# Kernel optimization log

Hardware: AMD Instinct MI355X
Metric: run time of the kernel (lower is better)

Reference implementation:

```python
import jax, jax.numpy as jnp
import numpy as np
from jax import lax

D_MODEL = 1024
EXPAND = 2
D_INNER = EXPAND * D_MODEL          # 2048
HEADDIM = 64
NHEADS = D_INNER // HEADDIM         # 32
D_STATE = 128
D_CONV = 4
NGROUPS = 1
CONV_DIM = D_INNER + 2 * NGROUPS * D_STATE   # 2304
D_IN_PROJ = 2 * D_INNER + 2 * NGROUPS * D_STATE + NHEADS  # 4384
EPS = 1e-5
BSZ, SEQ = 4, 1024


def _layer_norm(x):
    mu = jnp.mean(x, -1, keepdims=True)
    v = jnp.var(x, -1, keepdims=True)
    return (x - mu) * lax.rsqrt(v + EPS)


def _smart_flip(X, mask):
    # reverse only the non-padded prefix of each sequence
    B, L, _ = X.shape
    lengths = jnp.sum(~mask, axis=1)                     # (B,)
    r = jnp.arange(L)[None, :]                           # (1,L)
    pos = jnp.where(r < lengths[:, None], lengths[:, None] - 1 - r, r)
    return jnp.take_along_axis(X, pos[:, :, None], axis=1)


def _mamba2(u, in_proj_w, conv_w, conv_b, dt_bias, A_log, D, norm_w, out_proj_w):
    B, L, _ = u.shape
    zxbcdt = jnp.einsum('bld,ed->ble', u, in_proj_w)     # (B,L,D_IN_PROJ)
    z = zxbcdt[..., :D_INNER]
    xBC = zxbcdt[..., D_INNER:D_INNER + CONV_DIM]
    dt = zxbcdt[..., D_INNER + CONV_DIM:]                # (B,L,H)
    dt = jax.nn.softplus(dt + dt_bias)
    # causal depthwise conv1d over time, then SiLU
    xc = jnp.transpose(xBC, (0, 2, 1))                   # (B,C,L)
    xc = jnp.pad(xc, ((0, 0), (0, 0), (D_CONV - 1, 0)))
    xc = lax.conv_general_dilated(xc, conv_w.reshape(CONV_DIM, 1, D_CONV), (1,), 'VALID',
                                  feature_group_count=CONV_DIM)
    xBC = jax.nn.silu(jnp.transpose(xc + conv_b[None, :, None], (0, 2, 1)))
    x = xBC[..., :D_INNER].reshape(B, L, NHEADS, HEADDIM)
    Bmat = xBC[..., D_INNER:D_INNER + D_STATE]           # (B,L,N)  (ngroups=1)
    Cmat = xBC[..., D_INNER + D_STATE:]                  # (B,L,N)
    A = -jnp.exp(A_log)                                  # (H,)
    dA = jnp.exp(dt * A)                                 # (B,L,H)

    def step(h, inp):
        dA_t, dt_t, x_t, B_t, C_t = inp
        # h: (B,H,P,N)
        h = h * dA_t[:, :, None, None] + (dt_t[:, :, None] * x_t)[..., None] * B_t[:, None, None, :]
        y = jnp.einsum('bhpn,bn->bhp', h, C_t)
        return h, y

    h0 = jnp.zeros((B, NHEADS, HEADDIM, D_STATE), u.dtype)
    xs = (jnp.moveaxis(dA, 1, 0), jnp.moveaxis(dt, 1, 0), jnp.moveaxis(x, 1, 0),
          jnp.moveaxis(Bmat, 1, 0), jnp.moveaxis(Cmat, 1, 0))
    _, ys = lax.scan(step, h0, xs)                       # (L,B,H,P)
    y = jnp.moveaxis(ys, 0, 1) + D[None, None, :, None] * x
    y = y.reshape(B, L, D_INNER)
    g = y * jax.nn.silu(z)                               # gated RMSNorm (norm_before_gate=False)
    y = g * lax.rsqrt(jnp.mean(g * g, -1, keepdims=True) + EPS) * norm_w
    return jnp.einsum('ble,de->bld', y, out_proj_w)


def setup_inputs() -> dict:
    key = jax.random.key(0)
    ks = jax.random.split(key, 16)
    dt_f = jax.random.uniform(ks[4], (NHEADS,), minval=0.001, maxval=0.1)
    dt_r = jax.random.uniform(ks[10], (NHEADS,), minval=0.001, maxval=0.1)
    inv_softplus = lambda d: d + jnp.log(-jnp.expm1(-d))
    return {
        'hidden_states': jax.random.normal(ks[0], (BSZ, SEQ, D_MODEL), jnp.float32),
        'src_key_padding_mask': jnp.zeros((BSZ, SEQ), jnp.bool_),
        'in_proj_w': jax.random.normal(ks[1], (D_IN_PROJ, D_MODEL), jnp.float32) / np.sqrt(D_MODEL),
        'out_proj_w': jax.random.normal(ks[2], (D_MODEL, D_INNER), jnp.float32) / np.sqrt(D_INNER),
        'conv_w_f': jax.random.normal(ks[3], (CONV_DIM, D_CONV), jnp.float32) / np.sqrt(D_CONV),
        'conv_b_f': jnp.zeros((CONV_DIM,), jnp.float32),
        'dt_bias_f': inv_softplus(dt_f),
        'A_log_f': jnp.log(jax.random.uniform(ks[5], (NHEADS,), minval=1.0, maxval=16.0)),
        'D_f': jnp.ones((NHEADS,), jnp.float32),
        'norm_w_f': jnp.ones((D_INNER,), jnp.float32),
        'conv_w_r': jax.random.normal(ks[9], (CONV_DIM, D_CONV), jnp.float32) / np.sqrt(D_CONV),
        'conv_b_r': jnp.zeros((CONV_DIM,), jnp.float32),
        'dt_bias_r': inv_softplus(dt_r),
        'A_log_r': jnp.log(jax.random.uniform(ks[11], (NHEADS,), minval=1.0, maxval=16.0)),
        'D_r': jnp.ones((NHEADS,), jnp.float32),
        'norm_w_r': jnp.ones((D_INNER,), jnp.float32),
    }


def reference(hidden_states, src_key_padding_mask, in_proj_w, out_proj_w,
              conv_w_f, conv_b_f, dt_bias_f, A_log_f, D_f, norm_w_f,
              conv_w_r, conv_b_r, dt_bias_r, A_log_r, D_r, norm_w_r):
    h = _layer_norm(hidden_states)
    out = _mamba2(h, in_proj_w, conv_w_f, conv_b_f, dt_bias_f, A_log_f, D_f, norm_w_f, out_proj_w)
    rev = _smart_flip(h, src_key_padding_mask)
    out_rev = _mamba2(rev, in_proj_w, conv_w_r, conv_b_r, dt_bias_r, A_log_r, D_r, norm_w_r, out_proj_w)
    out_rev = _smart_flip(out_rev, src_key_padding_mask)
    out = (out + out_rev) / 2
    return _layer_norm(out)
```

## Files before the change

### kernel.cpp

```cpp
#include <hip/hip_runtime.h>


#define BSZ 4
#define SEQ 1024
#define DMODEL 1024
#define DINNER 2048
#define NHEADS 32
#define HEADDIM 64
#define DSTATE 128
#define CONVDIM 2304
#define DPROJ 4384
#define DPROJ_PAD 4480
#define NTOK (BSZ*SEQ)
#define EPSF 1e-5f
#define CH 32
#define NCHK (SEQ/CH)

typedef float f32x4 __attribute__((ext_vector_type(4)));
typedef __bf16 bf16x8 __attribute__((ext_vector_type(8)));

__device__ __forceinline__ unsigned short f2bf(float f) {
  unsigned int x = __float_as_uint(f);
  unsigned int r = (x + 0x7fffu + ((x >> 16) & 1u)) >> 16;
  return (unsigned short)r;
}
__device__ __forceinline__ float bf2f(unsigned short u) {
  return __uint_as_float(((unsigned int)u) << 16);
}

__device__ __forceinline__ void async_load16(const void* g, void* l) {
  __builtin_amdgcn_global_load_lds(
      (const __attribute__((address_space(1))) void*)g,
      (__attribute__((address_space(3))) void*)l, 16, 0, 0);
}

#define W1N (DPROJ_PAD * DMODEL)
#define W2N (DMODEL * DINNER)
__global__ void k_convert(const float* __restrict__ w1, const float* __restrict__ w2,
                          unsigned short* __restrict__ o1, unsigned short* __restrict__ o2) {
  int idx = blockIdx.x * 256 + threadIdx.x;
  if (idx < W1N) {
    int row = idx >> 10, col = idx & 1023;
    float v = (row < DPROJ) ? w1[(size_t)row * DMODEL + col] : 0.f;
    o1[idx] = f2bf(v);
  } else {
    int k = idx - W1N;
    o2[k] = f2bf(w2[k]);
  }
}
__global__ void k_lengths(const unsigned char* __restrict__ mask, int* __restrict__ lengths) {
  int b = blockIdx.x, tid = threadIdx.x;
  int cnt = 0;
  for (int k = 0; k < 4; ++k)
    cnt += (mask[(size_t)b * SEQ + tid + k * 256] == 0) ? 1 : 0;
  for (int o = 32; o > 0; o >>= 1) cnt += __shfl_down(cnt, o);
  __shared__ int red[4];
  if ((tid & 63) == 0) red[tid >> 6] = cnt;
  __syncthreads();
  if (tid == 0) lengths[b] = red[0] + red[1] + red[2] + red[3];
}

__global__ __launch_bounds__(256) void k_ln_bf16(const float* __restrict__ in,
                                                 unsigned short* __restrict__ out) {
  int row = blockIdx.x, tid = threadIdx.x;
  float4 v = ((const float4*)(in + (size_t)row * DMODEL))[tid];
  float s = v.x + v.y + v.z + v.w;
  float ss = v.x * v.x + v.y * v.y + v.z * v.z + v.w * v.w;
  for (int o = 32; o > 0; o >>= 1) { s += __shfl_down(s, o); ss += __shfl_down(ss, o); }
  __shared__ float red[8];
  if ((tid & 63) == 0) { red[tid >> 6] = s; red[4 + (tid >> 6)] = ss; }
  __syncthreads();
  s = red[0] + red[1] + red[2] + red[3];
  ss = red[4] + red[5] + red[6] + red[7];
  float mu = s * (1.f / DMODEL);
  float var = ss * (1.f / DMODEL) - mu * mu;
  float rs = rsqrtf(var + EPSF);
  ushort4 o;
  o.x = f2bf((v.x - mu) * rs); o.y = f2bf((v.y - mu) * rs);
  o.z = f2bf((v.z - mu) * rs); o.w = f2bf((v.w - mu) * rs);
  ((ushort4*)(out + (size_t)row * DMODEL))[tid] = o;
}

__global__ __launch_bounds__(256) void k_ln_out(const unsigned short* __restrict__ in,
                                                float* __restrict__ out) {
  int row = blockIdx.x, tid = threadIdx.x;
  ushort4 u = ((const ushort4*)(in + (size_t)row * DMODEL))[tid];
  float4 v;
  v.x = bf2f(u.x); v.y = bf2f(u.y); v.z = bf2f(u.z); v.w = bf2f(u.w);
  float s = v.x + v.y + v.z + v.w;
  float ss = v.x * v.x + v.y * v.y + v.z * v.z + v.w * v.w;
  for (int o = 32; o > 0; o >>= 1) { s += __shfl_down(s, o); ss += __shfl_down(ss, o); }
  __shared__ float red[8];
  if ((tid & 63) == 0) { red[tid >> 6] = s; red[4 + (tid >> 6)] = ss; }
  __syncthreads();
  s = red[0] + red[1] + red[2] + red[3];
  ss = red[4] + red[5] + red[6] + red[7];
  float mu = s * (1.f / DMODEL);
  float var = ss * (1.f / DMODEL) - mu * mu;
  float rs = rsqrtf(var + EPSF);
  float4 o;
  o.x = (v.x - mu) * rs; o.y = (v.y - mu) * rs;
  o.z = (v.z - mu) * rs; o.w = (v.w - mu) * rs;
  ((float4*)(out + (size_t)row * DMODEL))[tid] = o;
}

__global__ __launch_bounds__(256) void k_gemm_bt_h(const unsigned short* __restrict__ A,
                                                   const unsigned short* __restrict__ B,
                                                   unsigned short* __restrict__ C,
                                                   int K, int lda, int ldb, int ldc) {
  __shared__ unsigned short Asm[2][128 * 32];
  __shared__ unsigned short Bsm[2][128 * 32];
  const int tid = threadIdx.x;
  const int lane = tid & 63;
  const int w = tid >> 6;
  const int wm = w >> 1, wn = w & 1;
  const long m0 = (long)blockIdx.x * 128;
  const long n0 = (long)blockIdx.y * 128;

  const int sr = lane >> 2;
  const int sc = (lane & 3) * 8;
  const unsigned short* gA0 = A + (m0 + (w * 2 + 0) * 16 + sr) * (long)lda + sc;
  const unsigned short* gA1 = A + (m0 + (w * 2 + 1) * 16 + sr) * (long)lda + sc;
  const unsigned short* gB0 = B + (n0 + (w * 2 + 0) * 16 + sr) * (long)ldb + sc;
  const unsigned short* gB1 = B + (n0 + (w * 2 + 1) * 16 + sr) * (long)ldb + sc;

  f32x4 acc[4][4] = {};
  const int q8 = (lane >> 4) * 8;
  const int r16 = lane & 15;

  for (int k0 = 0; k0 < K; k0 += 64) {
#pragma unroll
    for (int h = 0; h < 2; ++h) {
      const int ko = k0 + h * 32;
      async_load16(gA0 + ko, Asm[h] + (w * 2 + 0) * 512);
      async_load16(gA1 + ko, Asm[h] + (w * 2 + 1) * 512);
      async_load16(gB0 + ko, Bsm[h] + (w * 2 + 0) * 512);
      async_load16(gB1 + ko, Bsm[h] + (w * 2 + 1) * 512);
    }
    __syncthreads();
#pragma unroll
    for (int h = 0; h < 2; ++h) {
      bf16x8 af[4], bfr[4];
#pragma unroll
      for (int i = 0; i < 4; ++i)
        af[i] = *reinterpret_cast<const bf16x8*>(Asm[h] + (wm * 64 + i * 16 + r16) * 32 + q8);
#pragma unroll
      for (int j = 0; j < 4; ++j)
        bfr[j] = *reinterpret_cast<const bf16x8*>(Bsm[h] + (wn * 64 + j * 16 + r16) * 32 + q8);
#pragma unroll
      for (int i = 0; i < 4; ++i)
#pragma unroll
        for (int j = 0; j < 4; ++j)
          acc[i][j] = __builtin_amdgcn_mfma_f32_16x16x32_bf16(af[i], bfr[j], acc[i][j], 0, 0, 0);
    }
    __syncthreads();
  }
  const int q = lane >> 4, cn = lane & 15;
#pragma unroll
  for (int i = 0; i < 4; ++i)
#pragma unroll
    for (int j = 0; j < 4; ++j) {
      long crow = m0 + wm * 64 + i * 16 + q * 4;
      long ccol = n0 + wn * 64 + j * 16 + cn;
#pragma unroll
      for (int r = 0; r < 4; ++r)
        C[(crow + r) * (long)ldc + ccol] = f2bf(acc[i][j][r]);
    }
}

__global__ __launch_bounds__(256) void k_conv(
    const __bf16* __restrict__ zxb,
    const float* __restrict__ cw_f, const float* __restrict__ cb_f,
    const float* __restrict__ cw_r, const float* __restrict__ cb_r,
    const int* __restrict__ lengths,
    __bf16* __restrict__ xb) {
  const int bx = blockIdx.x;
  const int tg = bx & 63;
  const int db = bx >> 6;
  const int b = db & 3;
  const int dir = db >> 2;
  const int tid = threadIdx.x;
  const int len = lengths[b];
  const int t0 = tg * 16;

  const float* cw = dir ? cw_r : cw_f;
  const float* cb = dir ? cb_r : cb_f;

  float w0[9], w1[9], w2[9], w3[9], bias[9];
  float r0[9], r1[9], r2[9], r3[9];
#pragma unroll
  for (int k = 0; k < 9; ++k) {
    int c = tid + k * 256;
    float4 w4 = *(const float4*)(cw + (size_t)c * 4);
    w0[k] = w4.x; w1[k] = w4.y; w2[k] = w4.z; w3[k] = w4.w;
    bias[k] = cb[c];
    r0[k] = 0.f; r1[k] = 0.f; r2[k] = 0.f;
  }
  auto rowptr = [&](int tt) -> const __bf16* {
    int s = dir ? ((tt < len) ? (len - 1 - tt) : tt) : tt;
    return zxb + ((size_t)b * SEQ + s) * DPROJ_PAD + DINNER;
  };
  if (t0 >= 3) {
    const __bf16* ra = rowptr(t0 - 3);
    const __bf16* rb = rowptr(t0 - 2);
    const __bf16* rc = rowptr(t0 - 1);
#pragma unroll
    for (int k = 0; k < 9; ++k) {
      int c = tid + k * 256;
      r0[k] = (float)ra[c]; r1[k] = (float)rb[c]; r2[k] = (float)rc[c];
    }
  }
  {
    const __bf16* rp = rowptr(t0);
#pragma unroll
    for (int k = 0; k < 9; ++k) r3[k] = (float)rp[tid + k * 256];
  }
  for (int j = 0; j < 16; ++j) {
    float r4[9];
    if (j < 15) {
      const __bf16* rp = rowptr(t0 + j + 1);
#pragma unroll
      for (int k = 0; k < 9; ++k) r4[k] = (float)rp[tid + k * 256];
    }
    __bf16* orow = xb + ((size_t)db * SEQ + t0 + j) * CONVDIM;
#pragma unroll
    for (int k = 0; k < 9; ++k) {
      float acc = bias[k];
      acc = fmaf(w0[k], r0[k], acc);
      acc = fmaf(w1[k], r1[k], acc);
      acc = fmaf(w2[k], r2[k], acc);
      acc = fmaf(w3[k], r3[k], acc);
      float sig = 1.f / (1.f + __expf(-acc));
      orow[tid + k * 256] = (__bf16)(acc * sig);
      r0[k] = r1[k]; r1[k] = r2[k]; r2[k] = r3[k]; r3[k] = r4[k];
    }
  }
}

__global__ __launch_bounds__(256) void k_dtprep(
    const __bf16* __restrict__ zxb,
    const float* __restrict__ dtb_f, const float* __restrict__ dtb_r,
    const float* __restrict__ al_f, const float* __restrict__ al_r,
    const int* __restrict__ lengths, float* __restrict__ ddg) {
  const int task = (blockIdx.x * 256 + threadIdx.x) >> 5;
  const int l32 = threadIdx.x & 31;
  const int chunk = task & 31, hh = (task >> 5) & 31, db = task >> 10;
  const int b = db & 3, dir = db >> 2;
  const int len = lengths[b];
  const float dtbv = (dir ? dtb_r : dtb_f)[hh];
  const float Ah = -__expf((dir ? al_r : al_f)[hh]);
  const int s = chunk * 32 + l32;
  const int sf = dir ? ((s < len) ? (len - 1 - s) : s) : s;
  float raw = (float)zxb[(size_t)(b * SEQ + sf) * DPROJ_PAD + DINNER + CONVDIM + hh] + dtbv;
  float d = (raw > 20.f) ? raw : log1pf(__expf(raw));
  float cum = d;
#pragma unroll
  for (int o = 1; o < 32; o <<= 1) {
    float v = __shfl_up(cum, o, 32);
    if (l32 >= o) cum += v;
  }
  float cum31 = __shfl(cum, 31, 32);
  float* o = ddg + (size_t)task * 128;
  o[l32]      = d;
  o[32 + l32] = Ah * cum;
  o[64 + l32] = d * __expf(Ah * (cum31 - cum));
  o[96 + l32] = __expf(Ah * cum);
}

__global__ __launch_bounds__(256, 2) void k_scan(
    const __bf16* __restrict__ xb, const float* __restrict__ ddg,
    const float* __restrict__ D_f, const float* __restrict__ D_r,
    unsigned short* __restrict__ y) {
  __shared__ __bf16 Crawf[4096];
  __shared__ __bf16 Brawf[4096];
  __shared__ __bf16 Braw2[4096];
  __shared__ __bf16 BTf[4096];
  __shared__ float  ddL[2][128];
  __shared__ __bf16 SL[1024];
  __shared__ __bf16 HL[4][2048];
  __shared__ __bf16 yO[2][32 * 72];

  const int bx = blockIdx.x;
  const int h = bx & 31;
  const int db = bx >> 5;
  const int dir = db >> 2;
  const int tid = threadIdx.x;
  const int lane = tid & 63;
  const int w = tid >> 6;
  const int l15 = lane & 15;
  const int q = lane >> 4;

  const float Dh = (dir ? D_r : D_f)[h];
  const __bf16* xbase = xb + (size_t)db * SEQ * CONVDIM;
  const float* ddbase = ddg + (size_t)bx * NCHK * 128;
  unsigned short* ybase = y + (size_t)db * SEQ * DINNER + h * HEADDIM;

  for (int i = lane; i < 2048; i += 64) HL[w][i] = (__bf16)0.f;
  for (int i = tid; i < 1024; i += 256) SL[i] = (__bf16)0.f;

  f32x4 accH[8] = {};

  auto issue = [&](int c, int nb) {
    const __bf16* xr = xbase + (size_t)c * CH * CONVDIM;
#pragma unroll
    for (int k = 0; k < 2; ++k) {
      const int idx = w * 2 + k;
      const int P = idx * 64 + lane;
      const int tt = P >> 8, kk = (P >> 6) & 3, qq = (P >> 4) & 3, ll = P & 15;
      const __bf16* gB = xr + (size_t)(tt * 16 + ll) * CONVDIM + DINNER + kk * 32 + qq * 8;
      async_load16(gB, &Brawf[idx * 512]);
      async_load16(gB + 128, &Crawf[idx * 512]);
      const int s = P >> 4, n8 = P & 15;
      const __bf16* g2 = xr + (size_t)s * CONVDIM + DINNER + n8 * 8;
      async_load16(g2, &Braw2[idx * 512]);
    }
    if (w == 3 && lane < 32)
      async_load16(ddbase + (size_t)c * 128 + lane * 4, &ddL[nb][0]);
  };

  auto load_xt = [&](int c) {
    bf16x8 v;
    const __bf16* gx = xbase + (size_t)(c * CH + q * 8) * CONVDIM + h * HEADDIM + w * 16 + l15;
#pragma unroll
    for (int j = 0; j < 8; ++j) v[j] = gx[(size_t)j * CONVDIM];
    return v;
  };

  issue(0, 0);
  bf16x8 xt = load_xt(0);
  __syncthreads();

  for (int c = 0; c < NCHK; ++c) {
    const int cb = c & 1, nb = cb ^ 1;

    if (c > 0) {
      const int tf = tid >> 3, p8 = (tid & 7) * 8;
      bf16x8 vy = *(const bf16x8*)&yO[nb][tf * 72 + p8];
      *(bf16x8*)(ybase + (size_t)((c - 1) * CH + tf) * DINNER + p8) = vy;
    }

    {
      const int n = tid & 127, sg = tid >> 7;
#pragma unroll
      for (int e = 0; e < 2; ++e) {
        const int qp = sg * 2 + e;
        bf16x8 v;
#pragma unroll
        for (int j = 0; j < 8; ++j) v[j] = Braw2[(qp * 8 + j) * 128 + n];
        *(bf16x8*)&BTf[((n >> 4) * 64 + qp * 16 + (n & 15)) * 8] = v;
      }
    }

    bf16x8 Cf0[4], Cf1[4];
#pragma unroll
    for (int kk = 0; kk < 4; ++kk) {
      Cf0[kk] = *(const bf16x8*)&Crawf[(kk * 64 + lane) * 8];
      Cf1[kk] = *(const bf16x8*)&Crawf[((4 + kk) * 64 + lane) * 8];
    }
    if (w < 3) {
      const int tt = (w == 0) ? 0 : 1;
      const int ss = (w == 2) ? 1 : 0;
      f32x4 G = {};
#pragma unroll
      for (int kk = 0; kk < 4; ++kk) {
        bf16x8 Bq = *(const bf16x8*)&Brawf[((ss * 4 + kk) * 64 + lane) * 8];
        G = __builtin_amdgcn_mfma_f32_16x16x32_bf16(tt ? Cf1[kk] : Cf0[kk], Bq, G, 0, 0, 0);
      }
      const int sgl = ss * 16 + l15;
      const float sdt = ddL[cb][sgl];
      const float scd = ddL[cb][32 + sgl];
#pragma unroll
      for (int r = 0; r < 4; ++r) {
        const int t0 = q * 4 + r;
        float v = G[r] * sdt * __expf(ddL[cb][32 + tt * 16 + t0] - scd);
        if (tt == ss) {
          if (t0 < l15) v = 0.f;
          else if (t0 == l15) v += Dh;
        }
        SL[(tt * 64 + (ss * 2 + (l15 >> 3)) * 16 + t0) * 8 + (l15 & 7)] = (__bf16)v;
      }
    }
    __syncthreads();

    if (c + 1 < NCHK) issue(c + 1, nb);
    bf16x8 xt_n;
    if (c + 1 < NCHK) xt_n = load_xt(c + 1);

    f32x4 accy0 = {}, accy1 = {};
    {
      bf16x8 S0 = *(const bf16x8*)&SL[(lane) * 8];
      bf16x8 S1 = *(const bf16x8*)&SL[(64 + lane) * 8];
      accy0 = __builtin_amdgcn_mfma_f32_16x16x32_bf16(xt, S0, accy0, 0, 0, 0);
      accy1 = __builtin_amdgcn_mfma_f32_16x16x32_bf16(xt, S1, accy1, 0, 0, 0);
    }
    {
      f32x4 ai0 = {}, ai1 = {};
#pragma unroll
      for (int kk = 0; kk < 4; ++kk) {
        bf16x8 Hf = *(const bf16x8*)&HL[w][(kk * 64 + lane) * 8];
        ai0 = __builtin_amdgcn_mfma_f32_16x16x32_bf16(Hf, Cf0[kk], ai0, 0, 0, 0);
        ai1 = __builtin_amdgcn_mfma_f32_16x16x32_bf16(Hf, Cf1[kk], ai1, 0, 0, 0);
      }
      const float P0 = ddL[cb][96 + l15], P1 = ddL[cb][96 + 16 + l15];
      accy0 = accy0 + ai0 * P0;
      accy1 = accy1 + ai1 * P1;
    }
    {
      const float atot = ddL[cb][96 + 31];
      bf16x8 xw;
#pragma unroll
      for (int j = 0; j < 8; ++j)
        xw[j] = (__bf16)((float)xt[j] * ddL[cb][64 + q * 8 + j]);
#pragma unroll
      for (int nt = 0; nt < 8; ++nt) {
        bf16x8 Bt = *(const bf16x8*)&BTf[(nt * 64 + lane) * 8];
        accH[nt] = accH[nt] * atot;
        accH[nt] = __builtin_amdgcn_mfma_f32_16x16x32_bf16(xw, Bt, accH[nt], 0, 0, 0);
      }
#pragma unroll
      for (int nt = 0; nt < 8; ++nt)
#pragma unroll
        for (int r = 0; r < 4; ++r) {
          const int n = nt * 16 + l15;
          HL[w][((n >> 5) * 64 + ((n & 31) >> 3) * 16 + q * 4 + r) * 8 + (n & 7)] =
              (__bf16)accH[nt][r];
        }
    }
#pragma unroll
    for (int r = 0; r < 4; ++r) {
      const int p = w * 16 + q * 4 + r;
      yO[cb][l15 * 72 + p]        = (__bf16)accy0[r];
      yO[cb][(16 + l15) * 72 + p] = (__bf16)accy1[r];
    }
    xt = xt_n;
    __syncthreads();
  }
  {
    const int tf = tid >> 3, p8 = (tid & 7) * 8;
    bf16x8 vy = *(const bf16x8*)&yO[(NCHK - 1) & 1][tf * 72 + p8];
    *(bf16x8*)(ybase + (size_t)((NCHK - 1) * CH + tf) * DINNER + p8) = vy;
  }
}

__global__ __launch_bounds__(256) void k_gate_combine(
    const __bf16* __restrict__ zxb, const unsigned short* __restrict__ y,
    const float* __restrict__ nw_f, const float* __restrict__ nw_r,
    const int* __restrict__ lengths, unsigned short* __restrict__ comb) {
  const int bx = blockIdx.x;
  const int b = bx >> 10, l = bx & 1023;
  const int tid = threadIdx.x;
  const int len = lengths[b];
  const int pos = (l < len) ? (len - 1 - l) : l;
  const __bf16* z = zxb + (size_t)bx * DPROJ_PAD;
  const unsigned short* yf = y + ((size_t)b * SEQ + l) * DINNER;
  const unsigned short* yr = y + ((size_t)(BSZ + b) * SEQ + pos) * DINNER;

  float gf[8], gr[8];
  float sf = 0.f, sr = 0.f;
#pragma unroll
  for (int k = 0; k < 8; ++k) {
    int c = tid + k * 256;
    float zz = (float)z[c];
    float sz = zz / (1.f + __expf(-zz));
    float vf = bf2f(yf[c]) * sz;
    float vr = bf2f(yr[c]) * sz;
    gf[k] = vf; gr[k] = vr;
    sf += vf * vf; sr += vr * vr;
  }
  for (int o = 32; o > 0; o >>= 1) { sf += __shfl_down(sf, o); sr += __shfl_down(sr, o); }
  __shared__ float red[8];
  if ((tid & 63) == 0) { red[tid >> 6] = sf; red[4 + (tid >> 6)] = sr; }
  __syncthreads();
  sf = red[0] + red[1] + red[2] + red[3];
  sr = red[4] + red[5] + red[6] + red[7];
  float rf = rsqrtf(sf * (1.f / DINNER) + EPSF);
  float rr = rsqrtf(sr * (1.f / DINNER) + EPSF);
#pragma unroll
  for (int k = 0; k < 8; ++k) {
    int c = tid + k * 256;
    float o = 0.5f * (gf[k] * rf * nw_f[c] + gr[k] * rr * nw_r[c]);
    comb[(size_t)bx * DINNER + c] = f2bf(o);
  }
}

extern "C" void kernel_launch(void* const* d_in, const int* in_sizes, int n_in,
                              void* d_out, int out_size, void* d_ws, size_t ws_size,
                              hipStream_t stream) {
  const float* hidden      = (const float*)d_in[0];
  const unsigned char* msk = (const unsigned char*)d_in[1];
  const float* in_proj_w   = (const float*)d_in[2];
  const float* out_proj_w  = (const float*)d_in[3];
  const float* conv_w_f    = (const float*)d_in[4];
  const float* conv_b_f    = (const float*)d_in[5];
  const float* dt_bias_f   = (const float*)d_in[6];
  const float* A_log_f     = (const float*)d_in[7];
  const float* D_f         = (const float*)d_in[8];
  const float* norm_w_f    = (const float*)d_in[9];
  const float* conv_w_r    = (const float*)d_in[10];
  const float* conv_b_r    = (const float*)d_in[11];
  const float* dt_bias_r   = (const float*)d_in[12];
  const float* A_log_r     = (const float*)d_in[13];
  const float* D_r         = (const float*)d_in[14];
  const float* norm_w_r    = (const float*)d_in[15];
  float* outF = (float*)d_out;

  char* ws = (char*)d_ws;
  size_t o_w1b  = 0;
  size_t o_w2b  = o_w1b  + 9175040;
  size_t o_hb   = o_w2b  + 4194304;
  size_t o_zx   = o_hb   + 8388608;
  size_t o_xb   = o_zx   + 36700160;
  size_t o_dd   = o_xb   + 37748736;
  size_t o_y    = o_dd   + 4194304;
  size_t o_comb = o_y    + 33554432;
  size_t o_outp = o_comb + 16777216;
  size_t o_len  = o_outp + 8388608;

  unsigned short* W1b  = (unsigned short*)(ws + o_w1b);
  unsigned short* W2b  = (unsigned short*)(ws + o_w2b);
  unsigned short* hb   = (unsigned short*)(ws + o_hb);
  __bf16*         zxb  = (__bf16*)(ws + o_zx);
  __bf16*         xb   = (__bf16*)(ws + o_xb);
  float*          ddg  = (float*)(ws + o_dd);
  unsigned short* yB   = (unsigned short*)(ws + o_y);
  unsigned short* comb = (unsigned short*)(ws + o_comb);
  unsigned short* outp = (unsigned short*)(ws + o_outp);
  int*            lens = (int*)(ws + o_len);

  k_convert<<<(W1N + W2N) / 256, 256, 0, stream>>>(in_proj_w, out_proj_w, W1b, W2b);
  k_lengths<<<BSZ, 256, 0, stream>>>(msk, lens);

  k_ln_bf16<<<NTOK, 256, 0, stream>>>(hidden, hb);

  k_gemm_bt_h<<<dim3(NTOK / 128, DPROJ_PAD / 128), 256, 0, stream>>>(
      hb, W1b, (unsigned short*)zxb, DMODEL, DMODEL, DMODEL, DPROJ_PAD);

  k_conv<<<2 * BSZ * (SEQ / 16), 256, 0, stream>>>(
      zxb, conv_w_f, conv_b_f, conv_w_r, conv_b_r, lens, xb);

  k_dtprep<<<1024, 256, 0, stream>>>(
      zxb, dt_bias_f, dt_bias_r, A_log_f, A_log_r, lens, ddg);

  k_scan<<<2 * BSZ * NHEADS, 256, 0, stream>>>(xb, ddg, D_f, D_r, yB);

  k_gate_combine<<<NTOK, 256, 0, stream>>>(zxb, yB, norm_w_f, norm_w_r, lens, comb);

  k_gemm_bt_h<<<dim3(NTOK / 128, DMODEL / 128), 256, 0, stream>>>(
      comb, W2b, outp, DINNER, DINNER, DINNER, DMODEL);

  k_ln_out<<<NTOK, 256, 0, stream>>>(outp, outF);

  (void)in_sizes; (void)n_in; (void)out_size; (void)ws_size;
}
```

Before: 312.1 us.

## Emit transposed B matrix from conv kernel and load it directly in scan

```diff
diff --git a/kernel.cpp b/kernel.cpp
--- a/kernel.cpp
+++ b/kernel.cpp
@@ -18,6 +18,7 @@
 
 typedef float f32x4 __attribute__((ext_vector_type(4)));
 typedef __bf16 bf16x8 __attribute__((ext_vector_type(8)));
+typedef __bf16 bf16x4 __attribute__((ext_vector_type(4)));
 
 __device__ __forceinline__ unsigned short f2bf(float f) {
   unsigned int x = __float_as_uint(f);
@@ -173,7 +174,7 @@
     const float* __restrict__ cw_f, const float* __restrict__ cb_f,
     const float* __restrict__ cw_r, const float* __restrict__ cb_r,
     const int* __restrict__ lengths,
-    __bf16* __restrict__ xb) {
+    __bf16* __restrict__ xb, __bf16* __restrict__ xbt) {
   const int bx = blockIdx.x;
   const int tg = bx & 63;
   const int db = bx >> 6;
@@ -215,6 +216,8 @@
 #pragma unroll
     for (int k = 0; k < 9; ++k) r3[k] = (float)rp[tid + k * 256];
   }
+  __bf16* btrow = (tid < 128) ? (xbt + ((size_t)db * 128 + tid) * SEQ + t0) : nullptr;
+
   for (int j = 0; j < 16; ++j) {
     float r4[9];
     if (j < 15) {
@@ -231,7 +234,9 @@
       acc = fmaf(w2[k], r2[k], acc);
       acc = fmaf(w3[k], r3[k], acc);
       float sig = 1.f / (1.f + __expf(-acc));
-      orow[tid + k * 256] = (__bf16)(acc * sig);
+      __bf16 ov = (__bf16)(acc * sig);
+      orow[tid + k * 256] = ov;
+      if (k == 8 && tid < 128) btrow[j] = ov;
       r0[k] = r1[k]; r1[k] = r2[k]; r2[k] = r3[k]; r3[k] = r4[k];
     }
   }
@@ -268,13 +273,13 @@
 }
 
 __global__ __launch_bounds__(256, 2) void k_scan(
-    const __bf16* __restrict__ xb, const float* __restrict__ ddg,
+    const __bf16* __restrict__ xb, const __bf16* __restrict__ xbt,
+    const float* __restrict__ ddg,
     const float* __restrict__ D_f, const float* __restrict__ D_r,
     unsigned short* __restrict__ y) {
   __shared__ __bf16 Crawf[4096];
   __shared__ __bf16 Brawf[4096];
-  __shared__ __bf16 Braw2[4096];
-  __shared__ __bf16 BTf[4096];
+  __shared__ __bf16 BTf[2][4096];
   __shared__ float  ddL[2][128];
   __shared__ __bf16 SL[1024];
   __shared__ __bf16 HL[4][2048];
@@ -292,6 +297,7 @@
 
   const float Dh = (dir ? D_r : D_f)[h];
   const __bf16* xbase = xb + (size_t)db * SEQ * CONVDIM;
+  const __bf16* xtbase = xbt + (size_t)db * 128 * SEQ;
   const float* ddbase = ddg + (size_t)bx * NCHK * 128;
   unsigned short* ybase = y + (size_t)db * SEQ * DINNER + h * HEADDIM;
 
@@ -310,9 +316,8 @@
       const __bf16* gB = xr + (size_t)(tt * 16 + ll) * CONVDIM + DINNER + kk * 32 + qq * 8;
       async_load16(gB, &Brawf[idx * 512]);
       async_load16(gB + 128, &Crawf[idx * 512]);
-      const int s = P >> 4, n8 = P & 15;
-      const __bf16* g2 = xr + (size_t)s * CONVDIM + DINNER + n8 * 8;
-      async_load16(g2, &Braw2[idx * 512]);
+      const __bf16* gT = xtbase + (size_t)(idx * 16 + l15) * SEQ + c * CH + q * 8;
+      async_load16(gT, &BTf[nb][idx * 512]);
     }
     if (w == 3 && lane < 32)
       async_load16(ddbase + (size_t)c * 128 + lane * 4, &ddL[nb][0]);
@@ -337,18 +342,6 @@
       const int tf = tid >> 3, p8 = (tid & 7) * 8;
       bf16x8 vy = *(const bf16x8*)&yO[nb][tf * 72 + p8];
       *(bf16x8*)(ybase + (size_t)((c - 1) * CH + tf) * DINNER + p8) = vy;
-    }
-
-    {
-      const int n = tid & 127, sg = tid >> 7;
-#pragma unroll
-      for (int e = 0; e < 2; ++e) {
-        const int qp = sg * 2 + e;
-        bf16x8 v;
-#pragma unroll
-        for (int j = 0; j < 8; ++j) v[j] = Braw2[(qp * 8 + j) * 128 + n];
-        *(bf16x8*)&BTf[((n >> 4) * 64 + qp * 16 + (n & 15)) * 8] = v;
-      }
     }
 
     bf16x8 Cf0[4], Cf1[4];
@@ -413,18 +406,18 @@
         xw[j] = (__bf16)((float)xt[j] * ddL[cb][64 + q * 8 + j]);
 #pragma unroll
       for (int nt = 0; nt < 8; ++nt) {
-        bf16x8 Bt = *(const bf16x8*)&BTf[(nt * 64 + lane) * 8];
+        bf16x8 Bt = *(const bf16x8*)&BTf[cb][(nt * 64 + lane) * 8];
         accH[nt] = accH[nt] * atot;
-        accH[nt] = __builtin_amdgcn_mfma_f32_16x16x32_bf16(xw, Bt, accH[nt], 0, 0, 0);
+        accH[nt] = __builtin_amdgcn_mfma_f32_16x16x32_bf16(Bt, xw, accH[nt], 0, 0, 0);
       }
 #pragma unroll
-      for (int nt = 0; nt < 8; ++nt)
-#pragma unroll
-        for (int r = 0; r < 4; ++r) {
-          const int n = nt * 16 + l15;
-          HL[w][((n >> 5) * 64 + ((n & 31) >> 3) * 16 + q * 4 + r) * 8 + (n & 7)] =
-              (__bf16)accH[nt][r];
-        }
+      for (int nt = 0; nt < 8; ++nt) {
+        const int n0 = nt * 16 + q * 4;
+        bf16x4 hv;
+#pragma unroll
+        for (int r = 0; r < 4; ++r) hv[r] = (__bf16)accH[nt][r];
+        *(bf16x4*)&HL[w][(n0 >> 5) * 512 + ((n0 >> 3) & 3) * 128 + l15 * 8 + (n0 & 7)] = hv;
+      }
     }
 #pragma unroll
     for (int r = 0; r < 4; ++r) {
@@ -515,6 +508,7 @@
   size_t o_comb = o_y    + 33554432;
   size_t o_outp = o_comb + 16777216;
   size_t o_len  = o_outp + 8388608;
+  size_t o_xbt  = o_len  + 256;
 
   unsigned short* W1b  = (unsigned short*)(ws + o_w1b);
   unsigned short* W2b  = (unsigned short*)(ws + o_w2b);
@@ -526,6 +520,7 @@
   unsigned short* comb = (unsigned short*)(ws + o_comb);
   unsigned short* outp = (unsigned short*)(ws + o_outp);
   int*            lens = (int*)(ws + o_len);
+  __bf16*         xbt  = (__bf16*)(ws + o_xbt);
 
   k_convert<<<(W1N + W2N) / 256, 256, 0, stream>>>(in_proj_w, out_proj_w, W1b, W2b);
   k_lengths<<<BSZ, 256, 0, stream>>>(msk, lens);
@@ -536,12 +531,12 @@
       hb, W1b, (unsigned short*)zxb, DMODEL, DMODEL, DMODEL, DPROJ_PAD);
 
   k_conv<<<2 * BSZ * (SEQ / 16), 256, 0, stream>>>(
-      zxb, conv_w_f, conv_b_f, conv_w_r, conv_b_r, lens, xb);
+      zxb, conv_w_f, conv_b_f, conv_w_r, conv_b_r, lens, xb, xbt);
 
   k_dtprep<<<1024, 256, 0, stream>>>(
       zxb, dt_bias_f, dt_bias_r, A_log_f, A_log_r, lens, ddg);
 
-  k_scan<<<2 * BSZ * NHEADS, 256, 0, stream>>>(xb, ddg, D_f, D_r, yB);
+  k_scan<<<2 * BSZ * NHEADS, 256, 0, stream>>>(xb, xbt, ddg, D_f, D_r, yB);
 
   k_gate_combine<<<NTOK, 256, 0, stream>>>(zxb, yB, norm_w_f, norm_w_r, lens, comb);
 
```

After: 319.6 us. 2.4% more time.

## Split scan headdim across two blocks of 128 threads for more parallelism

Applied to the files above, without the earlier changes.

```diff
diff --git a/kernel.cpp b/kernel.cpp
--- a/kernel.cpp
+++ b/kernel.cpp
@@ -18,6 +18,7 @@
 
 typedef float f32x4 __attribute__((ext_vector_type(4)));
 typedef __bf16 bf16x8 __attribute__((ext_vector_type(8)));
+typedef __bf16 bf16x4 __attribute__((ext_vector_type(4)));
 
 __device__ __forceinline__ unsigned short f2bf(float f) {
   unsigned int x = __float_as_uint(f);
@@ -267,7 +268,7 @@
   o[96 + l32] = __expf(Ah * cum);
 }
 
-__global__ __launch_bounds__(256, 2) void k_scan(
+__global__ __launch_bounds__(128) void k_scan(
     const __bf16* __restrict__ xb, const float* __restrict__ ddg,
     const float* __restrict__ D_f, const float* __restrict__ D_r,
     unsigned short* __restrict__ y) {
@@ -277,12 +278,14 @@
   __shared__ __bf16 BTf[4096];
   __shared__ float  ddL[2][128];
   __shared__ __bf16 SL[1024];
-  __shared__ __bf16 HL[4][2048];
-  __shared__ __bf16 yO[2][32 * 72];
-
-  const int bx = blockIdx.x;
-  const int h = bx & 31;
-  const int db = bx >> 5;
+  __shared__ __bf16 HL[2][2048];
+  __shared__ __bf16 yO[2][32 * 40];
+
+  const int bxi = blockIdx.x;
+  const int half = bxi >> 8;
+  const int task = bxi & 255;
+  const int h = task & 31;
+  const int db = task >> 5;
   const int dir = db >> 2;
   const int tid = threadIdx.x;
   const int lane = tid & 63;
@@ -292,19 +295,19 @@
 
   const float Dh = (dir ? D_r : D_f)[h];
   const __bf16* xbase = xb + (size_t)db * SEQ * CONVDIM;
-  const float* ddbase = ddg + (size_t)bx * NCHK * 128;
-  unsigned short* ybase = y + (size_t)db * SEQ * DINNER + h * HEADDIM;
+  const float* ddbase = ddg + (size_t)task * NCHK * 128;
+  unsigned short* ybase = y + (size_t)db * SEQ * DINNER + h * HEADDIM + half * 32;
 
   for (int i = lane; i < 2048; i += 64) HL[w][i] = (__bf16)0.f;
-  for (int i = tid; i < 1024; i += 256) SL[i] = (__bf16)0.f;
+  for (int i = tid; i < 1024; i += 128) SL[i] = (__bf16)0.f;
 
   f32x4 accH[8] = {};
 
   auto issue = [&](int c, int nb) {
     const __bf16* xr = xbase + (size_t)c * CH * CONVDIM;
 #pragma unroll
-    for (int k = 0; k < 2; ++k) {
-      const int idx = w * 2 + k;
+    for (int k = 0; k < 4; ++k) {
+      const int idx = w * 4 + k;
       const int P = idx * 64 + lane;
       const int tt = P >> 8, kk = (P >> 6) & 3, qq = (P >> 4) & 3, ll = P & 15;
       const __bf16* gB = xr + (size_t)(tt * 16 + ll) * CONVDIM + DINNER + kk * 32 + qq * 8;
@@ -314,13 +317,14 @@
       const __bf16* g2 = xr + (size_t)s * CONVDIM + DINNER + n8 * 8;
       async_load16(g2, &Braw2[idx * 512]);
     }
-    if (w == 3 && lane < 32)
+    if (w == 1 && lane < 32)
       async_load16(ddbase + (size_t)c * 128 + lane * 4, &ddL[nb][0]);
   };
 
   auto load_xt = [&](int c) {
     bf16x8 v;
-    const __bf16* gx = xbase + (size_t)(c * CH + q * 8) * CONVDIM + h * HEADDIM + w * 16 + l15;
+    const __bf16* gx = xbase + (size_t)(c * CH + q * 8) * CONVDIM + h * HEADDIM
+                       + half * 32 + w * 16 + l15;
 #pragma unroll
     for (int j = 0; j < 8; ++j) v[j] = gx[(size_t)j * CONVDIM];
     return v;
@@ -334,20 +338,19 @@
     const int cb = c & 1, nb = cb ^ 1;
 
     if (c > 0) {
-      const int tf = tid >> 3, p8 = (tid & 7) * 8;
-      bf16x8 vy = *(const bf16x8*)&yO[nb][tf * 72 + p8];
+      const int tf = tid >> 2, p8 = (tid & 3) * 8;
+      bf16x8 vy = *(const bf16x8*)&yO[nb][tf * 40 + p8];
       *(bf16x8*)(ybase + (size_t)((c - 1) * CH + tf) * DINNER + p8) = vy;
     }
 
     {
-      const int n = tid & 127, sg = tid >> 7;
-#pragma unroll
-      for (int e = 0; e < 2; ++e) {
-        const int qp = sg * 2 + e;
+      const int n = tid;
+#pragma unroll
+      for (int e = 0; e < 4; ++e) {
         bf16x8 v;
 #pragma unroll
-        for (int j = 0; j < 8; ++j) v[j] = Braw2[(qp * 8 + j) * 128 + n];
-        *(bf16x8*)&BTf[((n >> 4) * 64 + qp * 16 + (n & 15)) * 8] = v;
+        for (int j = 0; j < 8; ++j) v[j] = Braw2[(e * 8 + j) * 128 + n];
+        *(bf16x8*)&BTf[((n >> 4) * 64 + e * 16 + (n & 15)) * 8] = v;
       }
     }
 
@@ -357,27 +360,30 @@
       Cf0[kk] = *(const bf16x8*)&Crawf[(kk * 64 + lane) * 8];
       Cf1[kk] = *(const bf16x8*)&Crawf[((4 + kk) * 64 + lane) * 8];
     }
-    if (w < 3) {
-      const int tt = (w == 0) ? 0 : 1;
-      const int ss = (w == 2) ? 1 : 0;
-      f32x4 G = {};
-#pragma unroll
-      for (int kk = 0; kk < 4; ++kk) {
-        bf16x8 Bq = *(const bf16x8*)&Brawf[((ss * 4 + kk) * 64 + lane) * 8];
-        G = __builtin_amdgcn_mfma_f32_16x16x32_bf16(tt ? Cf1[kk] : Cf0[kk], Bq, G, 0, 0, 0);
-      }
-      const int sgl = ss * 16 + l15;
-      const float sdt = ddL[cb][sgl];
-      const float scd = ddL[cb][32 + sgl];
-#pragma unroll
-      for (int r = 0; r < 4; ++r) {
-        const int t0 = q * 4 + r;
-        float v = G[r] * sdt * __expf(ddL[cb][32 + tt * 16 + t0] - scd);
-        if (tt == ss) {
-          if (t0 < l15) v = 0.f;
-          else if (t0 == l15) v += Dh;
+    {
+      const int nG = (w == 0) ? 2 : 1;
+      for (int g = 0; g < nG; ++g) {
+        const int tt = (w == 0) ? g : 1;
+        const int ss = (w == 0) ? g : 0;
+        f32x4 G = {};
+#pragma unroll
+        for (int kk = 0; kk < 4; ++kk) {
+          bf16x8 Bq = *(const bf16x8*)&Brawf[((ss * 4 + kk) * 64 + lane) * 8];
+          G = __builtin_amdgcn_mfma_f32_16x16x32_bf16(tt ? Cf1[kk] : Cf0[kk], Bq, G, 0, 0, 0);
         }
-        SL[(tt * 64 + (ss * 2 + (l15 >> 3)) * 16 + t0) * 8 + (l15 & 7)] = (__bf16)v;
+        const int sgl = ss * 16 + l15;
+        const float sdt = ddL[cb][sgl];
+        const float scd = ddL[cb][32 + sgl];
+#pragma unroll
+        for (int r = 0; r < 4; ++r) {
+          const int t0 = q * 4 + r;
+          float v = G[r] * sdt * __expf(ddL[cb][32 + tt * 16 + t0] - scd);
+          if (tt == ss) {
+            if (t0 < l15) v = 0.f;
+            else if (t0 == l15) v += Dh;
+          }
+          SL[(tt * 64 + (ss * 2 + (l15 >> 3)) * 16 + t0) * 8 + (l15 & 7)] = (__bf16)v;
+        }
       }
     }
     __syncthreads();
@@ -429,15 +435,15 @@
 #pragma unroll
     for (int r = 0; r < 4; ++r) {
       const int p = w * 16 + q * 4 + r;
-      yO[cb][l15 * 72 + p]        = (__bf16)accy0[r];
-      yO[cb][(16 + l15) * 72 + p] = (__bf16)accy1[r];
+      yO[cb][l15 * 40 + p]        = (__bf16)accy0[r];
+      yO[cb][(16 + l15) * 40 + p] = (__bf16)accy1[r];
     }
     xt = xt_n;
     __syncthreads();
   }
   {
-    const int tf = tid >> 3, p8 = (tid & 7) * 8;
-    bf16x8 vy = *(const bf16x8*)&yO[(NCHK - 1) & 1][tf * 72 + p8];
+    const int tf = tid >> 2, p8 = (tid & 3) * 8;
+    bf16x8 vy = *(const bf16x8*)&yO[(NCHK - 1) & 1][tf * 40 + p8];
     *(bf16x8*)(ybase + (size_t)((NCHK - 1) * CH + tf) * DINNER + p8) = vy;
   }
 }
@@ -541,7 +547,7 @@
   k_dtprep<<<1024, 256, 0, stream>>>(
       zxb, dt_bias_f, dt_bias_r, A_log_f, A_log_r, lens, ddg);
 
-  k_scan<<<2 * BSZ * NHEADS, 256, 0, stream>>>(xb, ddg, D_f, D_r, yB);
+  k_scan<<<2 * 2 * BSZ * NHEADS, 128, 0, stream>>>(xb, ddg, D_f, D_r, yB);
 
   k_gate_combine<<<NTOK, 256, 0, stream>>>(zxb, yB, norm_w_f, norm_w_r, lens, comb);
 
```

New measurement: 334.7 us. 7.2% more time.
